# Kernel optimization log

Hardware: AMD Instinct MI355X
Metric: run time of the kernel (lower is better)

## Reference

```python
import jax, jax.numpy as jnp
import numpy as np

N = 50000
E = 500000
IN_DIM = 128
HID = 128
EDGE_DIM = 1
MAX_DEPTH = 4  # depth values in [0, MAX_DEPTH]


def setup_inputs() -> dict:
    key = jax.random.key(0)
    ks = jax.random.split(key, 10)
    x = jax.random.normal(ks[0], (N, IN_DIM), jnp.float32)
    edge_index = jax.random.randint(ks[1], (2, E), 0, N)
    edge_attr = jax.random.normal(ks[2], (E, EDGE_DIM), jnp.float32)
    depth = jax.random.randint(ks[3], (N,), 0, MAX_DEPTH + 1)
    def w(k, sh):
        return (jax.random.normal(k, sh, jnp.float32) / np.float32(np.sqrt(sh[0])))
    return {
        "x": x, "edge_index": edge_index, "edge_attr": edge_attr, "depth": depth,
        "pw": w(ks[4], (IN_DIM, HID)), "pb": jnp.zeros((HID,), jnp.float32),
        "mw1": w(ks[5], (HID + EDGE_DIM, HID)), "mb1": jnp.zeros((HID,), jnp.float32),
        "mw2": w(ks[6], (HID, HID)), "mb2": jnp.zeros((HID,), jnp.float32),
        "uw1": w(ks[7], (2 * HID, HID)), "ub1": jnp.zeros((HID,), jnp.float32),
        "uw2": w(ks[8], (HID, HID)), "ub2": jnp.zeros((HID,), jnp.float32),
    }


def reference(x, edge_index, edge_attr, depth, pw, pb, mw1, mb1, mw2, mb2, uw1, ub1, uw2, ub2):
    src, dst = edge_index[0], edge_index[1]
    dst_depth = depth[dst]  # [E]
    h = x @ pw + pb  # node_proj -> [N, HID]
    # Sequential topological DP over depth levels (static unroll, small count).
    for d in range(1, MAX_DEPTH + 1):
        emask = dst_depth == d  # [E]
        # msg_mlp over all edges using current h (lower-depth nodes already updated)
        msg_in = jnp.concatenate([h[src], edge_attr], axis=-1)  # [E, HID+EDGE_DIM]
        msgs = jax.nn.relu(jax.nn.relu(msg_in @ mw1 + mb1) @ mw2 + mb2)
        msgs = jnp.where(emask[:, None], msgs, jnp.zeros((), h.dtype))
        agg = jax.ops.segment_sum(msgs, dst, num_segments=N)  # [N, HID]
        counts = jax.ops.segment_sum(emask.astype(h.dtype), dst, num_segments=N)
        agg = agg / jnp.clip(counts, 1.0)[:, None]  # mean aggregation, clamp(min=1)
        upd_in = jnp.concatenate([h, agg], axis=-1)  # [N, 2*HID]
        h_new = jax.nn.relu(jax.nn.relu(upd_in @ uw1 + ub1) @ uw2 + ub2)
        h = jnp.where((depth == d)[:, None], h_new, h)
    return h
```

## Files before the change

kernel.cpp:

```cpp
#include <hip/hip_runtime.h>

typedef _Float16 f16;
typedef f16 f16x2 __attribute__((ext_vector_type(2)));
typedef f16 f16x8 __attribute__((ext_vector_type(8)));
typedef float f32x4 __attribute__((ext_vector_type(4)));
typedef float f32x2 __attribute__((ext_vector_type(2)));

#define MFMA16(a, b, c) __builtin_amdgcn_mfma_f32_16x16x32_f16((a), (b), (c), 0, 0, 0)

static __device__ __forceinline__ f16x8 cvt8(const float* __restrict__ p) {
    f32x4 p0 = *(const f32x4*)p;
    f32x4 p1 = *(const f32x4*)(p + 4);
    f16x8 a;
    a[0] = (f16)p0[0]; a[1] = (f16)p0[1]; a[2] = (f16)p0[2]; a[3] = (f16)p0[3];
    a[4] = (f16)p1[0]; a[5] = (f16)p1[1]; a[6] = (f16)p1[2]; a[7] = (f16)p1[3];
    return a;
}

__global__ __launch_bounds__(256) void k_prep(
        const float* __restrict__ pw, const float* __restrict__ mw1,
        const float* __restrict__ mw2, const float* __restrict__ uw1,
        const float* __restrict__ uw2,
        f16* __restrict__ pwp, f16* __restrict__ mw1p, f16* __restrict__ mw2p,
        f16* __restrict__ uw1p, f16* __restrict__ uw2p,
        const int* __restrict__ ei, int* __restrict__ degv,
        const int* __restrict__ dep, int* __restrict__ dcnt,
        int4* __restrict__ recs, int CB, int E, int N) {
    __shared__ int lcnt[4];
    __shared__ int lbase[4];
    int b = blockIdx.x;
    int t = threadIdx.x;
    if (b < 48) {
        const float* W; f16* out; int fb;
        if (b < 8)       { W = pw;  out = pwp;  fb = b; }
        else if (b < 16) { W = mw1; out = mw1p; fb = b - 8; }
        else if (b < 24) { W = mw2; out = mw2p; fb = b - 16; }
        else if (b < 40) { W = uw1; out = uw1p; fb = b - 24; }
        else             { W = uw2; out = uw2p; fb = b - 40; }
        int idx = fb * 256 + t;
        int lane = idx & 63;
        int nt = (idx >> 6) & 7;
        int kt = idx >> 9;
        int colx = lane & 15, quad = lane >> 4;
        f16* o = out + (size_t)idx * 8;
        const float* wb = W + (size_t)(kt * 32 + quad * 8) * 128 + nt * 16 + colx;
#pragma unroll
        for (int j = 0; j < 8; j++) o[j] = (f16)wb[(size_t)j * 128];
    } else if (b < 48 + CB) {
        int e = (b - 48) * 256 + t;
        if (e < E) atomicAdd(&degv[ei[E + e]], 1);
    } else {
        if (t < 4) lcnt[t] = 0;
        __syncthreads();
        int v = (b - 48 - CB) * 256 + t;
        int d = (v < N) ? dep[v] : 0;
        int p = -1;
        if (d >= 1 && d <= 4) p = atomicAdd(&lcnt[d - 1], 1);
        __syncthreads();
        if (t < 4) lbase[t] = (lcnt[t] > 0) ? atomicAdd(&dcnt[t], lcnt[t]) : 0;
        __syncthreads();
        if (d >= 1 && d <= 4) recs[(size_t)(d - 1) * N + lbase[d - 1] + p].x = v;
    }
}

__global__ __launch_bounds__(256) void k_mid(
        const int* __restrict__ degv, int* __restrict__ bsum, int SB,
        const float* __restrict__ x, const f16* __restrict__ pwp,
        const f16* __restrict__ mw1p, const float* __restrict__ pb,
        const float* __restrict__ mb1, float* __restrict__ h,
        f16* __restrict__ hh, f16* __restrict__ t, int N) {
    __shared__ __align__(16) f16 lds[4][16 * 136];
    __shared__ int wsum[4];
    int tid = threadIdx.x;
    if ((int)blockIdx.x < SB) {
        int idx = blockIdx.x * 256 + tid;
        int v = (idx < N) ? degv[idx] : 0;
#pragma unroll
        for (int off = 32; off; off >>= 1) v += __shfl_down(v, off, 64);
        if ((tid & 63) == 0) wsum[tid >> 6] = v;
        __syncthreads();
        if (tid == 0) bsum[blockIdx.x] = wsum[0] + wsum[1] + wsum[2] + wsum[3];
        return;
    }
    int lane = tid & 63, w = tid >> 6;
    int colx = lane & 15, quad = lane >> 4;
    int base = ((blockIdx.x - SB) * 4 + w) * 16;
    int arow = base + colx;
    int u = arow < N ? arow : N - 1;

    f32x4 c1[8];
#pragma unroll
    for (int nt = 0; nt < 8; nt++) c1[nt] = (f32x4){0.f, 0.f, 0.f, 0.f};
#pragma unroll
    for (int kt = 0; kt < 4; kt++) {
        f16x8 a = cvt8(x + (size_t)u * 128 + kt * 32 + quad * 8);
#pragma unroll
        for (int nt = 0; nt < 8; nt++) {
            f16x8 b = *(const f16x8*)(pwp + ((size_t)(kt * 8 + nt) * 64 + lane) * 8);
            c1[nt] = MFMA16(a, b, c1[nt]);
        }
    }
#pragma unroll
    for (int nt = 0; nt < 8; nt++) {
        float bias = pb[nt * 16 + colx];
#pragma unroll
        for (int reg = 0; reg < 4; reg++) {
            int row = quad * 4 + reg;
            int node = base + row;
            float v = c1[nt][reg] + bias;
            lds[w][row * 136 + nt * 16 + colx] = (f16)v;
            if (node < N) {
                h[(size_t)node * 128 + nt * 16 + colx] = v;
                hh[(size_t)node * 128 + nt * 16 + colx] = (f16)v;
            }
        }
    }
    f32x4 c2[8];
#pragma unroll
    for (int nt = 0; nt < 8; nt++) c2[nt] = (f32x4){0.f, 0.f, 0.f, 0.f};
#pragma unroll
    for (int kt = 0; kt < 4; kt++) {
        f16x8 a = *(const f16x8*)&lds[w][colx * 136 + kt * 32 + quad * 8];
#pragma unroll
        for (int nt = 0; nt < 8; nt++) {
            f16x8 b = *(const f16x8*)(mw1p + ((size_t)(kt * 8 + nt) * 64 + lane) * 8);
            c2[nt] = MFMA16(a, b, c2[nt]);
        }
    }
#pragma unroll
    for (int nt = 0; nt < 8; nt++) {
        float bias = mb1[nt * 16 + colx];
#pragma unroll
        for (int reg = 0; reg < 4; reg++) {
            int node = base + quad * 4 + reg;
            if (node < N) t[(size_t)node * 128 + nt * 16 + colx] = (f16)(c2[nt][reg] + bias);
        }
    }
}

__global__ __launch_bounds__(256) void k_scanC(const int* __restrict__ degv,
                                               const int* __restrict__ bsum,
                                               int* __restrict__ rowp, int N, int E) {
    __shared__ int lds[256];
    __shared__ int wo[4];
    int b = blockIdx.x, t = threadIdx.x;
    int idx = b * 256 + t;
    int v = (idx < N) ? degv[idx] : 0;
    lds[t] = v;
    __syncthreads();
#pragma unroll
    for (int d = 1; d < 256; d <<= 1) {
        int u = (t >= d) ? lds[t - d] : 0;
        __syncthreads();
        lds[t] += u;
        __syncthreads();
    }
    int off = 0;
    for (int j = t; j < b; j += 256) off += bsum[j];
#pragma unroll
    for (int o = 32; o; o >>= 1) off += __shfl_down(off, o, 64);
    if ((t & 63) == 0) wo[t >> 6] = off;
    __syncthreads();
    int boff = wo[0] + wo[1] + wo[2] + wo[3];
    if (idx < N) rowp[idx] = boff + lds[t] - v;
    if (b == 0 && t == 0) rowp[N] = E;
}

__global__ __launch_bounds__(256) void k_scat(const int* __restrict__ ei,
                                              const float* __restrict__ eattr,
                                              const int* __restrict__ dep,
                                              const int* __restrict__ rowp,
                                              int* __restrict__ cur,
                                              int2* __restrict__ esea,
                                              int4* __restrict__ recs,
                                              const int* __restrict__ dcnt,
                                              int E, int N) {
    int gtid = blockIdx.x * 256 + threadIdx.x;
    int gsz = gridDim.x * 256;
    for (int e = gtid; e < E; e += gsz) {
        int s = ei[e], d = ei[E + e];
        int p = rowp[d] + atomicAdd(&cur[d], 1);
        esea[p] = (int2){s | (dep[s] << 20), __float_as_int(eattr[e])};
    }
    for (int d4 = 0; d4 < 4; d4++) {
        int cnt = dcnt[d4];
        for (int i = gtid; i < cnt; i += gsz) {
            int4* r = &recs[(size_t)d4 * N + i];
            int u = r->x;
            r->y = rowp[u];
            r->z = rowp[u + 1];
        }
    }
}

__global__ __launch_bounds__(256) void k_md(
        const f16* __restrict__ tOrg, f16* __restrict__ tUpd,
        const float* __restrict__ mw1, const float* __restrict__ mb2,
        const f16* __restrict__ mw2p, const int2* __restrict__ esea,
        const int4* __restrict__ recs, const int* __restrict__ dcnt,
        const f16* __restrict__ hh, const f16* __restrict__ uw1p,
        const f16* __restrict__ uw2p, const f16* __restrict__ mw1p,
        const float* __restrict__ ub1, const float* __restrict__ ub2,
        const float* __restrict__ mb1, float* __restrict__ h,
        int dIdx, int N) {
    __shared__ __align__(16) f16 bsm[128 * 128];
    __shared__ __align__(16) f16 tbuf[4][16][136];
    __shared__ int2 ebuf[4][16];
    __shared__ __align__(16) f16 pool[16][136];
    __shared__ __align__(16) f16 sout[16][136];
    __shared__ int ids[16], se0[16], se1[16];
    {
        const f16x8* s8 = (const f16x8*)mw2p;
        f16x8* d8 = (f16x8*)bsm;
        for (int i = threadIdx.x; i < 2048; i += 256) d8[i] = s8[i];
    }

    const int tid = threadIdx.x;
    const int lane = tid & 63;
    const int w = tid >> 6;
    const int colx = lane & 15, quad = lane >> 4;
    const int cnt = dcnt[dIdx];

    const float* w1r = mw1 + 128 * 128;
    f16x8 w1h[4];
#pragma unroll
    for (int kt = 0; kt < 4; kt++) {
        f32x4 q0 = *(const f32x4*)(w1r + kt * 32 + quad * 8);
        f32x4 q1 = *(const f32x4*)(w1r + kt * 32 + quad * 8 + 4);
        w1h[kt][0] = (f16)q0[0]; w1h[kt][1] = (f16)q0[1];
        w1h[kt][2] = (f16)q0[2]; w1h[kt][3] = (f16)q0[3];
        w1h[kt][4] = (f16)q1[0]; w1h[kt][5] = (f16)q1[1];
        w1h[kt][6] = (f16)q1[2]; w1h[kt][7] = (f16)q1[3];
    }
    float mb2v[8];
#pragma unroll
    for (int nt = 0; nt < 8; nt++) mb2v[nt] = mb2[nt * 16 + colx];

    const int b = blockIdx.x, nb = gridDim.x;
    const int s0 = (int)((long long)cnt * b / nb);
    const int s1 = (int)((long long)cnt * (b + 1) / nb);
    f16* hb = &tbuf[0][0][0];

    __syncthreads();

    for (int cs = s0; cs < s1; cs += 16) {
        int cc = s1 - cs; if (cc > 16) cc = 16;
        if (tid < 16) {
            if (tid < cc) {
                int4 r = recs[(size_t)dIdx * N + cs + tid];
                ids[tid] = r.x; se0[tid] = r.y; se1[tid] = r.z;
            } else {
                ids[tid] = 0; se0[tid] = 0; se1[tid] = 0;
            }
        }
        __syncthreads();

        for (int q = 0; q < 4; q++) {
            int maxT = 0;
#pragma unroll
            for (int s = 0; s < 4; s++) {
                int r = q * 4 + s;
                int tc = (se1[r] - se0[r] + 15) >> 4;
                if (tc > maxT) maxT = tc;
            }
            float aggv[8] = {0.f, 0.f, 0.f, 0.f, 0.f, 0.f, 0.f, 0.f};
            for (int rd = 0; rd < maxT; rd++) {
                if (tid < 64) {
                    int s = tid >> 4, j = tid & 15;
                    int r = q * 4 + s;
                    int es = se0[r] + rd * 16 + j;
                    if (es < se1[r]) ebuf[s][j] = esea[es];
                }
                __syncthreads();
#pragma unroll
                for (int it = 0; it < 4; it++) {
                    int task = it * 256 + tid;
                    int row = task >> 4, seg = task & 15;
                    int s = row >> 4, j = row & 15;
                    int r = q * 4 + s;
                    int es = se0[r] + rd * 16 + j;
                    if (es < se1[r]) {
                        int sv = ebuf[s][j].x;
                        const f16* tb =
                            ((unsigned)((sv >> 20) - 1) < (unsigned)dIdx) ? tUpd : tOrg;
                        *(f16x8*)&tbuf[s][j][seg * 8] =
                            *(const f16x8*)(tb + (size_t)(sv & 0xFFFFF) * 128 + seg * 8);
                    }
                }
                __syncthreads();
                {
                    int r = q * 4 + w;
                    int bs = se0[r] + rd * 16;
                    int rem = se1[r] - bs;
                    if (rem > 0) {
                        f16 eah = (f16)__int_as_float(ebuf[w][colx].y);
                        f16x8 afr[4];
#pragma unroll
                        for (int kt = 0; kt < 4; kt++) {
                            f16x8 v = *(const f16x8*)&tbuf[w][colx][kt * 32 + quad * 8];
                            f16x8 o;
#pragma unroll
                            for (int j2 = 0; j2 < 8; j2++) {
                                f16 qv = v[j2] + eah * w1h[kt][j2];
                                o[j2] = qv > (f16)0 ? qv : (f16)0;
                            }
                            afr[kt] = o;
                        }
#pragma unroll
                        for (int nt = 0; nt < 8; nt++) {
                            f32x4 c = (f32x4){0.f, 0.f, 0.f, 0.f};
#pragma unroll
                            for (int kt = 0; kt < 4; kt++) {
                                f16x8 bb = *(const f16x8*)&bsm[((kt * 8 + nt) * 64 + lane) * 8];
                                c = MFMA16(afr[kt], bb, c);
                            }
#pragma unroll
                            for (int reg = 0; reg < 4; reg++)
                                if (quad * 4 + reg < rem)
                                    aggv[nt] += fmaxf(c[reg] + mb2v[nt], 0.f);
                        }
                    }
                }
                __syncthreads();
            }
            {
                int r = q * 4 + w;
                int deg = se1[r] - se0[r];
                float inv = 1.f / (float)(deg > 1 ? deg : 1);
#pragma unroll
                for (int nt = 0; nt < 8; nt++) {
                    float s = aggv[nt];
                    s += __shfl_xor(s, 16, 64);
                    s += __shfl_xor(s, 32, 64);
                    if (quad == 0) pool[r][nt * 16 + colx] = (f16)(s * inv);
                }
            }
        }
        __syncthreads();

        {
            int row = tid >> 4, seg = tid & 15;
            if (row < cc)
                *(f16x8*)&hb[row * 136 + seg * 8] =
                    *(const f16x8*)(hh + (size_t)ids[row] * 128 + seg * 8);
        }
        __syncthreads();

        f32x4 c1[2];
        c1[0] = (f32x4){0.f, 0.f, 0.f, 0.f};
        c1[1] = (f32x4){0.f, 0.f, 0.f, 0.f};
#pragma unroll
        for (int kt = 0; kt < 8; kt++) {
            f16x8 a;
            if (kt < 4)
                a = *(const f16x8*)&hb[colx * 136 + kt * 32 + quad * 8];
            else
                a = *(const f16x8*)&pool[colx][(kt - 4) * 32 + quad * 8];
#pragma unroll
            for (int j = 0; j < 2; j++) {
                int nt = 2 * w + j;
                f16x8 bb = *(const f16x8*)(uw1p + ((size_t)(kt * 8 + nt) * 64 + lane) * 8);
                c1[j] = MFMA16(a, bb, c1[j]);
            }
        }
#pragma unroll
        for (int j = 0; j < 2; j++) {
            int nt = 2 * w + j;
            float bias = ub1[nt * 16 + colx];
#pragma unroll
            for (int reg = 0; reg < 4; reg++) {
                int row = quad * 4 + reg;
                sout[row][nt * 16 + colx] = (f16)fmaxf(c1[j][reg] + bias, 0.f);
            }
        }
        __syncthreads();
        f32x4 c2[2];
        c2[0] = (f32x4){0.f, 0.f, 0.f, 0.f};
        c2[1] = (f32x4){0.f, 0.f, 0.f, 0.f};
#pragma unroll
        for (int kt = 0; kt < 4; kt++) {
            f16x8 a = *(const f16x8*)&sout[colx][kt * 32 + quad * 8];
#pragma unroll
            for (int j = 0; j < 2; j++) {
                int nt = 2 * w + j;
                f16x8 bb = *(const f16x8*)(uw2p + ((size_t)(kt * 8 + nt) * 64 + lane) * 8);
                c2[j] = MFMA16(a, bb, c2[j]);
            }
        }
#pragma unroll
        for (int j = 0; j < 2; j++) {
            int nt = 2 * w + j;
            float bias = ub2[nt * 16 + colx];
#pragma unroll
            for (int reg = 0; reg < 4; reg++) {
                int row = quad * 4 + reg;
                float v = fmaxf(c2[j][reg] + bias, 0.f);
                pool[row][nt * 16 + colx] = (f16)v;
                if (row < cc)
                    h[(size_t)ids[row] * 128 + nt * 16 + colx] = v;
            }
        }
        __syncthreads();
        if (dIdx < 3) {
            f32x4 c3[2];
            c3[0] = (f32x4){0.f, 0.f, 0.f, 0.f};
            c3[1] = (f32x4){0.f, 0.f, 0.f, 0.f};
#pragma unroll
            for (int kt = 0; kt < 4; kt++) {
                f16x8 a = *(const f16x8*)&pool[colx][kt * 32 + quad * 8];
#pragma unroll
                for (int j = 0; j < 2; j++) {
                    int nt = 2 * w + j;
                    f16x8 bb = *(const f16x8*)(mw1p + ((size_t)(kt * 8 + nt) * 64 + lane) * 8);
                    c3[j] = MFMA16(a, bb, c3[j]);
                }
            }
#pragma unroll
            for (int j = 0; j < 2; j++) {
                int nt = 2 * w + j;
                float bias = mb1[nt * 16 + colx];
#pragma unroll
                for (int reg = 0; reg < 4; reg++) {
                    int row = quad * 4 + reg;
                    if (row < cc)
                        tUpd[(size_t)ids[row] * 128 + nt * 16 + colx] =
                            (f16)(c3[j][reg] + bias);
                }
            }
        }
        __syncthreads();
    }
}

extern "C" void kernel_launch(void* const* d_in, const int* in_sizes, int n_in,
                              void* d_out, int out_size, void* d_ws, size_t ws_size,
                              hipStream_t stream) {
    const float* x    = (const float*)d_in[0];
    const int*   ei   = (const int*)d_in[1];
    const float* eatt = (const float*)d_in[2];
    const int*   dep  = (const int*)d_in[3];
    const float* pw   = (const float*)d_in[4];
    const float* pb   = (const float*)d_in[5];
    const float* mw1  = (const float*)d_in[6];
    const float* mb1  = (const float*)d_in[7];
    const float* mw2  = (const float*)d_in[8];
    const float* mb2  = (const float*)d_in[9];
    const float* uw1  = (const float*)d_in[10];
    const float* ub1  = (const float*)d_in[11];
    const float* uw2  = (const float*)d_in[12];
    const float* ub2  = (const float*)d_in[13];
    float* h = (float*)d_out;

    int N = in_sizes[3];
    int E = in_sizes[1] / 2;
    int NB = (N + 255) / 256;
    int CB = (E + 255) / 256;

    char* ws = (char*)d_ws;
    size_t o = 0;
    auto alloc = [&](size_t bytes) -> char* {
        char* p = ws + o;
        o += (bytes + 255) & ~(size_t)255;
        return p;
    };
    f16*   t    = (f16*)alloc((size_t)N * 128 * 2);
    f16*   hh   = (f16*)alloc((size_t)N * 128 * 2);
    f16*   tUpd = (f16*)alloc((size_t)N * 128 * 2);
    char*  z0   = (char*)alloc(0);
    int*   degv = (int*)alloc((size_t)N * 4);
    int*   cur  = (int*)alloc((size_t)N * 4);
    int*   dcnt = (int*)alloc(64);
    size_t zbytes = (size_t)((char*)alloc(0) - z0);
    int*   rowp = (int*)alloc((size_t)(N + 1) * 4);
    int*   bsum = (int*)alloc((size_t)NB * 4);
    int2*  esea = (int2*)alloc((size_t)E * 8);
    int4*  recs = (int4*)alloc((size_t)4 * N * 16);
    f16*   pwp  = (f16*)alloc(128 * 128 * 2);
    f16*   mw1p = (f16*)alloc(128 * 128 * 2);
    f16*   mw2p = (f16*)alloc(128 * 128 * 2);
    f16*   uw1p = (f16*)alloc(256 * 128 * 2);
    f16*   uw2p = (f16*)alloc(128 * 128 * 2);

    hipMemsetAsync(z0, 0, zbytes, stream);

    k_prep<<<48 + CB + NB, 256, 0, stream>>>(pw, mw1, mw2, uw1, uw2,
                                             pwp, mw1p, mw2p, uw1p, uw2p,
                                             ei, degv, dep, dcnt, recs, CB, E, N);
    int PB = (N + 63) / 64;
    k_mid<<<NB + PB, 256, 0, stream>>>(degv, bsum, NB, x, pwp, mw1p, pb, mb1,
                                       h, hh, t, N);
    k_scanC<<<NB, 256, 0, stream>>>(degv, bsum, rowp, N, E);
    k_scat<<<CB, 256, 0, stream>>>(ei, eatt, dep, rowp, cur, esea, recs, dcnt, E, N);

    for (int d = 0; d < 4; d++) {
        k_md<<<512, 256, 0, stream>>>(t, tUpd, mw1, mb2, mw2p, esea, recs, dcnt,
                                      hh, uw1p, uw2p, mw1p, ub1, ub2, mb1, h,
                                      d, N);
    }
}
```

Measured before the change: 341.9 us.

## Restructure per-depth kernel: 512-thread blocks, batched 16-node edge gather with prefetch

Raises the block size to 512 threads on a 256-block grid. Each chunk of 16 nodes now gathers the first 16 incoming edges of all nodes at once into a 256-row shared tile, and the next chunk's edge records are prefetched while the current one is processed. Node rows for the update MLP are loaded in the same phase, which removes several barriers per round. Edges beyond the first 16 per node are read straight from global memory by each wave, skipping shared staging. The update and message-projection GEMMs are spread over 8 waves instead of 4. This cuts synchronisation and gather latency, at the cost of more shared memory and registers per block, lower occupancy, and uncoalesced global reads for high-degree nodes.

```diff
diff --git a/kernel.cpp b/kernel.cpp
--- a/kernel.cpp
+++ b/kernel.cpp
@@ -193,7 +193,7 @@
     }
 }
 
-__global__ __launch_bounds__(256) void k_md(
+__global__ __launch_bounds__(512) void k_md(
         const f16* __restrict__ tOrg, f16* __restrict__ tUpd,
         const float* __restrict__ mw1, const float* __restrict__ mb2,
         const f16* __restrict__ mw2p, const int2* __restrict__ esea,
@@ -204,22 +204,24 @@
         const float* __restrict__ mb1, float* __restrict__ h,
         int dIdx, int N) {
     __shared__ __align__(16) f16 bsm[128 * 128];
-    __shared__ __align__(16) f16 tbuf[4][16][136];
-    __shared__ int2 ebuf[4][16];
-    __shared__ __align__(16) f16 pool[16][136];
-    __shared__ __align__(16) f16 sout[16][136];
-    __shared__ int ids[16], se0[16], se1[16];
-    {
-        const f16x8* s8 = (const f16x8*)mw2p;
-        f16x8* d8 = (f16x8*)bsm;
-        for (int i = threadIdx.x; i < 2048; i += 256) d8[i] = s8[i];
-    }
+    __shared__ __align__(16) f16 tbuf[256 * 136];
+    __shared__ __align__(16) f16 hbuf[16 * 136];
+    __shared__ __align__(16) f16 pool[16 * 136];
+    __shared__ __align__(16) f16 sout[16 * 136];
+    __shared__ int idsA[64], se0A[64], se1A[64];
 
     const int tid = threadIdx.x;
     const int lane = tid & 63;
     const int w = tid >> 6;
     const int colx = lane & 15, quad = lane >> 4;
     const int cnt = dcnt[dIdx];
+
+    {
+        const f16x8* s8 = (const f16x8*)mw2p;
+        f16x8* d8 = (f16x8*)bsm;
+#pragma unroll
+        for (int i = 0; i < 4; i++) d8[i * 512 + tid] = s8[i * 512 + tid];
+    }
 
     const float* w1r = mw1 + 128 * 128;
     f16x8 w1h[4];
@@ -236,83 +238,134 @@
 #pragma unroll
     for (int nt = 0; nt < 8; nt++) mb2v[nt] = mb2[nt * 16 + colx];
 
+    const int trow = tid & 255;
+    const int thalf = tid >> 8;
+    const int tnode = trow >> 4;
+    const int tj = trow & 15;
+
     const int b = blockIdx.x, nb = gridDim.x;
     const int s0 = (int)((long long)cnt * b / nb);
     const int s1 = (int)((long long)cnt * (b + 1) / nb);
-    f16* hb = &tbuf[0][0][0];
-
-    __syncthreads();
-
-    for (int cs = s0; cs < s1; cs += 16) {
-        int cc = s1 - cs; if (cc > 16) cc = 16;
-        if (tid < 16) {
-            if (tid < cc) {
-                int4 r = recs[(size_t)dIdx * N + cs + tid];
-                ids[tid] = r.x; se0[tid] = r.y; se1[tid] = r.z;
+
+    auto srow = [&](int sv) -> const f16* {
+        const f16* tb = ((unsigned)((sv >> 20) - 1) < (unsigned)dIdx) ? tUpd : tOrg;
+        return tb + (size_t)(sv & 0xFFFFF) * 128;
+    };
+
+    for (int ss = s0; ss < s1; ss += 64) {
+        int scc = s1 - ss; if (scc > 64) scc = 64;
+        __syncthreads();
+        if (tid < 64) {
+            if (tid < scc) {
+                int4 r = recs[(size_t)dIdx * N + ss + tid];
+                idsA[tid] = r.x; se0A[tid] = r.y; se1A[tid] = r.z;
             } else {
-                ids[tid] = 0; se0[tid] = 0; se1[tid] = 0;
-            }
-        }
-        __syncthreads();
-
-        for (int q = 0; q < 4; q++) {
-            int maxT = 0;
-#pragma unroll
-            for (int s = 0; s < 4; s++) {
-                int r = q * 4 + s;
-                int tc = (se1[r] - se0[r] + 15) >> 4;
-                if (tc > maxT) maxT = tc;
-            }
-            float aggv[8] = {0.f, 0.f, 0.f, 0.f, 0.f, 0.f, 0.f, 0.f};
-            for (int rd = 0; rd < maxT; rd++) {
-                if (tid < 64) {
-                    int s = tid >> 4, j = tid & 15;
-                    int r = q * 4 + s;
-                    int es = se0[r] + rd * 16 + j;
-                    if (es < se1[r]) ebuf[s][j] = esea[es];
-                }
-                __syncthreads();
-#pragma unroll
-                for (int it = 0; it < 4; it++) {
-                    int task = it * 256 + tid;
-                    int row = task >> 4, seg = task & 15;
-                    int s = row >> 4, j = row & 15;
-                    int r = q * 4 + s;
-                    int es = se0[r] + rd * 16 + j;
-                    if (es < se1[r]) {
-                        int sv = ebuf[s][j].x;
-                        const f16* tb =
-                            ((unsigned)((sv >> 20) - 1) < (unsigned)dIdx) ? tUpd : tOrg;
-                        *(f16x8*)&tbuf[s][j][seg * 8] =
-                            *(const f16x8*)(tb + (size_t)(sv & 0xFFFFF) * 128 + seg * 8);
+                idsA[tid] = 0; se0A[tid] = 0; se1A[tid] = 0;
+            }
+        }
+        __syncthreads();
+        int nch = (scc + 15) >> 4;
+
+        int2 erec = (int2){0, 0};
+        {
+            int d0 = se1A[tnode] - se0A[tnode];
+            if (tj < d0) erec = esea[se0A[tnode] + tj];
+        }
+
+        for (int ci = 0; ci < nch; ci++) {
+            int cc = scc - ci * 16; if (cc > 16) cc = 16;
+            int gidx = ci * 16 + tnode;
+            int deg = se1A[gidx] - se0A[gidx];
+            bool tval = (tj < deg);
+            f16x8 tld[8];
+            if (tval) {
+                const f16* tr = srow(erec.x) + thalf * 64;
+#pragma unroll
+                for (int i = 0; i < 8; i++) tld[i] = *(const f16x8*)(tr + i * 8);
+            }
+            f16x8 hld;
+            if (tid < 256) {
+                int hrow = tid >> 4, hseg = tid & 15;
+                hld = *(const f16x8*)(hh + (size_t)idsA[ci * 16 + hrow] * 128 + hseg * 8);
+            }
+            int2 erecN = (int2){0, 0};
+            if (ci + 1 < nch) {
+                int g2 = (ci + 1) * 16 + tnode;
+                int d2 = se1A[g2] - se0A[g2];
+                if (tj < d2) erecN = esea[se0A[g2] + tj];
+            }
+            if (tval) {
+                f16* dst = &tbuf[trow * 136 + thalf * 64];
+#pragma unroll
+                for (int i = 0; i < 8; i++) *(f16x8*)(dst + i * 8) = tld[i];
+                if (thalf == 0) tbuf[trow * 136 + 128] = (f16)__int_as_float(erec.y);
+            }
+            if (tid < 256) {
+                int hrow = tid >> 4, hseg = tid & 15;
+                *(f16x8*)&hbuf[hrow * 136 + hseg * 8] = hld;
+            }
+            __syncthreads();
+
+#pragma unroll
+            for (int nn = 0; nn < 2; nn++) {
+                int n = 2 * w + nn;
+                int gi = ci * 16 + n;
+                int nd = se1A[gi] - se0A[gi];
+                float aggv[8] = {0.f, 0.f, 0.f, 0.f, 0.f, 0.f, 0.f, 0.f};
+                if (nd > 0) {
+                    f16 eah = tbuf[(n * 16 + colx) * 136 + 128];
+                    f16x8 afr[4];
+#pragma unroll
+                    for (int kt = 0; kt < 4; kt++) {
+                        f16x8 v = *(const f16x8*)&tbuf[(n * 16 + colx) * 136 + kt * 32 + quad * 8];
+                        f16x8 o;
+#pragma unroll
+                        for (int j2 = 0; j2 < 8; j2++) {
+                            f16 qv = v[j2] + eah * w1h[kt][j2];
+                            o[j2] = qv > (f16)0 ? qv : (f16)0;
+                        }
+                        afr[kt] = o;
                     }
-                }
-                __syncthreads();
-                {
-                    int r = q * 4 + w;
-                    int bs = se0[r] + rd * 16;
-                    int rem = se1[r] - bs;
-                    if (rem > 0) {
-                        f16 eah = (f16)__int_as_float(ebuf[w][colx].y);
-                        f16x8 afr[4];
+                    int rem0 = nd < 16 ? nd : 16;
+#pragma unroll
+                    for (int nt = 0; nt < 8; nt++) {
+                        f32x4 c = (f32x4){0.f, 0.f, 0.f, 0.f};
 #pragma unroll
                         for (int kt = 0; kt < 4; kt++) {
-                            f16x8 v = *(const f16x8*)&tbuf[w][colx][kt * 32 + quad * 8];
+                            f16x8 bb = *(const f16x8*)&bsm[((kt * 8 + nt) * 64 + lane) * 8];
+                            c = MFMA16(afr[kt], bb, c);
+                        }
+#pragma unroll
+                        for (int reg = 0; reg < 4; reg++)
+                            if (quad * 4 + reg < rem0)
+                                aggv[nt] += fmaxf(c[reg] + mb2v[nt], 0.f);
+                    }
+                    for (int bs = 16; bs < nd; bs += 16) {
+                        int lim = se1A[gi] - 1;
+                        int es = se0A[gi] + bs + colx; if (es > lim) es = lim;
+                        int2 er = esea[es];
+                        f16 eah2 = (f16)__int_as_float(er.y);
+                        const f16* trw = srow(er.x);
+                        f16x8 af2[4];
+#pragma unroll
+                        for (int kt = 0; kt < 4; kt++) {
+                            f16x8 v = *(const f16x8*)(trw + kt * 32 + quad * 8);
                             f16x8 o;
 #pragma unroll
                             for (int j2 = 0; j2 < 8; j2++) {
-                                f16 qv = v[j2] + eah * w1h[kt][j2];
+                                f16 qv = v[j2] + eah2 * w1h[kt][j2];
                                 o[j2] = qv > (f16)0 ? qv : (f16)0;
                             }
-                            afr[kt] = o;
+                            af2[kt] = o;
                         }
+                        int rem = nd - bs;
 #pragma unroll
                         for (int nt = 0; nt < 8; nt++) {
                             f32x4 c = (f32x4){0.f, 0.f, 0.f, 0.f};
 #pragma unroll
                             for (int kt = 0; kt < 4; kt++) {
                                 f16x8 bb = *(const f16x8*)&bsm[((kt * 8 + nt) * 64 + lane) * 8];
-                                c = MFMA16(afr[kt], bb, c);
+                                c = MFMA16(af2[kt], bb, c);
                             }
 #pragma unroll
                             for (int reg = 0; reg < 4; reg++)
@@ -321,114 +374,76 @@
                         }
                     }
                 }
-                __syncthreads();
-            }
-            {
-                int r = q * 4 + w;
-                int deg = se1[r] - se0[r];
-                float inv = 1.f / (float)(deg > 1 ? deg : 1);
+                float inv = 1.f / (float)(nd > 1 ? nd : 1);
 #pragma unroll
                 for (int nt = 0; nt < 8; nt++) {
                     float s = aggv[nt];
                     s += __shfl_xor(s, 16, 64);
                     s += __shfl_xor(s, 32, 64);
-                    if (quad == 0) pool[r][nt * 16 + colx] = (f16)(s * inv);
+                    if (quad == 0) pool[n * 136 + nt * 16 + colx] = (f16)(s * inv);
                 }
             }
-        }
-        __syncthreads();
-
-        {
-            int row = tid >> 4, seg = tid & 15;
-            if (row < cc)
-                *(f16x8*)&hb[row * 136 + seg * 8] =
-                    *(const f16x8*)(hh + (size_t)ids[row] * 128 + seg * 8);
-        }
-        __syncthreads();
-
-        f32x4 c1[2];
-        c1[0] = (f32x4){0.f, 0.f, 0.f, 0.f};
-        c1[1] = (f32x4){0.f, 0.f, 0.f, 0.f};
-#pragma unroll
-        for (int kt = 0; kt < 8; kt++) {
-            f16x8 a;
-            if (kt < 4)
-                a = *(const f16x8*)&hb[colx * 136 + kt * 32 + quad * 8];
-            else
-                a = *(const f16x8*)&pool[colx][(kt - 4) * 32 + quad * 8];
-#pragma unroll
-            for (int j = 0; j < 2; j++) {
-                int nt = 2 * w + j;
-                f16x8 bb = *(const f16x8*)(uw1p + ((size_t)(kt * 8 + nt) * 64 + lane) * 8);
-                c1[j] = MFMA16(a, bb, c1[j]);
-            }
-        }
-#pragma unroll
-        for (int j = 0; j < 2; j++) {
-            int nt = 2 * w + j;
-            float bias = ub1[nt * 16 + colx];
-#pragma unroll
-            for (int reg = 0; reg < 4; reg++) {
-                int row = quad * 4 + reg;
-                sout[row][nt * 16 + colx] = (f16)fmaxf(c1[j][reg] + bias, 0.f);
-            }
-        }
-        __syncthreads();
-        f32x4 c2[2];
-        c2[0] = (f32x4){0.f, 0.f, 0.f, 0.f};
-        c2[1] = (f32x4){0.f, 0.f, 0.f, 0.f};
-#pragma unroll
-        for (int kt = 0; kt < 4; kt++) {
-            f16x8 a = *(const f16x8*)&sout[colx][kt * 32 + quad * 8];
-#pragma unroll
-            for (int j = 0; j < 2; j++) {
-                int nt = 2 * w + j;
-                f16x8 bb = *(const f16x8*)(uw2p + ((size_t)(kt * 8 + nt) * 64 + lane) * 8);
-                c2[j] = MFMA16(a, bb, c2[j]);
-            }
-        }
-#pragma unroll
-        for (int j = 0; j < 2; j++) {
-            int nt = 2 * w + j;
-            float bias = ub2[nt * 16 + colx];
-#pragma unroll
-            for (int reg = 0; reg < 4; reg++) {
-                int row = quad * 4 + reg;
-                float v = fmaxf(c2[j][reg] + bias, 0.f);
-                pool[row][nt * 16 + colx] = (f16)v;
-                if (row < cc)
-                    h[(size_t)ids[row] * 128 + nt * 16 + colx] = v;
-            }
-        }
-        __syncthreads();
-        if (dIdx < 3) {
-            f32x4 c3[2];
-            c3[0] = (f32x4){0.f, 0.f, 0.f, 0.f};
-            c3[1] = (f32x4){0.f, 0.f, 0.f, 0.f};
+            __syncthreads();
+
+            f32x4 c1 = (f32x4){0.f, 0.f, 0.f, 0.f};
+#pragma unroll
+            for (int kt = 0; kt < 8; kt++) {
+                f16x8 a;
+                if (kt < 4)
+                    a = *(const f16x8*)&hbuf[colx * 136 + kt * 32 + quad * 8];
+                else
+                    a = *(const f16x8*)&pool[colx * 136 + (kt - 4) * 32 + quad * 8];
+                f16x8 bb = *(const f16x8*)(uw1p + ((size_t)(kt * 8 + w) * 64 + lane) * 8);
+                c1 = MFMA16(a, bb, c1);
+            }
+            {
+                float bias = ub1[w * 16 + colx];
+#pragma unroll
+                for (int reg = 0; reg < 4; reg++) {
+                    int row = quad * 4 + reg;
+                    sout[row * 136 + w * 16 + colx] = (f16)fmaxf(c1[reg] + bias, 0.f);
+                }
+            }
+            __syncthreads();
+            f32x4 c2 = (f32x4){0.f, 0.f, 0.f, 0.f};
 #pragma unroll
             for (int kt = 0; kt < 4; kt++) {
-                f16x8 a = *(const f16x8*)&pool[colx][kt * 32 + quad * 8];
-#pragma unroll
-                for (int j = 0; j < 2; j++) {
-                    int nt = 2 * w + j;
-                    f16x8 bb = *(const f16x8*)(mw1p + ((size_t)(kt * 8 + nt) * 64 + lane) * 8);
-                    c3[j] = MFMA16(a, bb, c3[j]);
+                f16x8 a = *(const f16x8*)&sout[colx * 136 + kt * 32 + quad * 8];
+                f16x8 bb = *(const f16x8*)(uw2p + ((size_t)(kt * 8 + w) * 64 + lane) * 8);
+                c2 = MFMA16(a, bb, c2);
+            }
+            {
+                float bias = ub2[w * 16 + colx];
+#pragma unroll
+                for (int reg = 0; reg < 4; reg++) {
+                    int row = quad * 4 + reg;
+                    float v = fmaxf(c2[reg] + bias, 0.f);
+                    pool[row * 136 + w * 16 + colx] = (f16)v;
+                    if (row < cc)
+                        h[(size_t)idsA[ci * 16 + row] * 128 + w * 16 + colx] = v;
                 }
             }
-#pragma unroll
-            for (int j = 0; j < 2; j++) {
-                int nt = 2 * w + j;
-                float bias = mb1[nt * 16 + colx];
+            __syncthreads();
+            if (dIdx < 3) {
+                f32x4 c3 = (f32x4){0.f, 0.f, 0.f, 0.f};
+#pragma unroll
+                for (int kt = 0; kt < 4; kt++) {
+                    f16x8 a = *(const f16x8*)&pool[colx * 136 + kt * 32 + quad * 8];
+                    f16x8 bb = *(const f16x8*)(mw1p + ((size_t)(kt * 8 + w) * 64 + lane) * 8);
+                    c3 = MFMA16(a, bb, c3);
+                }
+                float bias = mb1[w * 16 + colx];
 #pragma unroll
                 for (int reg = 0; reg < 4; reg++) {
                     int row = quad * 4 + reg;
                     if (row < cc)
-                        tUpd[(size_t)ids[row] * 128 + nt * 16 + colx] =
-                            (f16)(c3[j][reg] + bias);
+                        tUpd[(size_t)idsA[ci * 16 + row] * 128 + w * 16 + colx] =
+                            (f16)(c3[reg] + bias);
                 }
             }
-        }
-        __syncthreads();
+            __syncthreads();
+            erec = erecN;
+        }
     }
 }
 
@@ -493,7 +508,7 @@
     k_scat<<<CB, 256, 0, stream>>>(ei, eatt, dep, rowp, cur, esea, recs, dcnt, E, N);
 
     for (int d = 0; d < 4; d++) {
-        k_md<<<512, 256, 0, stream>>>(t, tUpd, mw1, mb2, mw2p, esea, recs, dcnt,
+        k_md<<<256, 512, 0, stream>>>(t, tUpd, mw1, mb2, mw2p, esea, recs, dcnt,
                                       hh, uw1p, uw2p, mw1p, ub1, ub2, mb1, h,
                                       d, N);
     }
```

Measured after the change: 470.1 us. 1.37x slower.

## Register-prefetch next node group's source rows and drop per-round edge syncs

Applied to the files above, without the earlier changes.

Restructures the message-aggregation loop in the depth kernel. Edge records for all 16 nodes of a chunk are loaded up front. Source-row gathers for the next group of four nodes are issued into registers while the current group computes, and then committed to a double-buffered LDS tile. Nodes with more than 16 edges now have each wave load its own extra rows directly from global memory, with no block barriers, which removes the old per-round maxT loop and its three __syncthreads. The LDS padding changes from 136 to 132 and sout shares space with the tile buffer. The cost is higher register pressure, and the overflow edges use uncoalesced direct loads.

```diff
diff --git a/kernel.cpp b/kernel.cpp
--- a/kernel.cpp
+++ b/kernel.cpp
@@ -204,22 +204,26 @@
         const float* __restrict__ mb1, float* __restrict__ h,
         int dIdx, int N) {
     __shared__ __align__(16) f16 bsm[128 * 128];
-    __shared__ __align__(16) f16 tbuf[4][16][136];
-    __shared__ int2 ebuf[4][16];
-    __shared__ __align__(16) f16 pool[16][136];
-    __shared__ __align__(16) f16 sout[16][136];
+    __shared__ __align__(16) f16 tbuf[2][4][16][132];
+    __shared__ __align__(16) f16 pool[16][132];
+    __shared__ int2 ebuf[16][16];
     __shared__ int ids[16], se0[16], se1[16];
-    {
-        const f16x8* s8 = (const f16x8*)mw2p;
-        f16x8* d8 = (f16x8*)bsm;
-        for (int i = threadIdx.x; i < 2048; i += 256) d8[i] = s8[i];
-    }
+    f16* hbuf = &tbuf[0][0][0][0];
+    f16* sout = &tbuf[1][0][0][0];
 
     const int tid = threadIdx.x;
     const int lane = tid & 63;
     const int w = tid >> 6;
     const int colx = lane & 15, quad = lane >> 4;
+    const int er0 = tid >> 4;
+    const int sg = tid & 15;
     const int cnt = dcnt[dIdx];
+
+    {
+        const f16x8* s8 = (const f16x8*)mw2p;
+        f16x8* d8 = (f16x8*)bsm;
+        for (int i = tid; i < 2048; i += 256) d8[i] = s8[i];
+    }
 
     const float* w1r = mw1 + 128 * 128;
     f16x8 w1h[4];
@@ -237,14 +241,33 @@
     for (int nt = 0; nt < 8; nt++) mb2v[nt] = mb2[nt * 16 + colx];
 
     const int b = blockIdx.x, nb = gridDim.x;
-    const int s0 = (int)((long long)cnt * b / nb);
-    const int s1 = (int)((long long)cnt * (b + 1) / nb);
-    f16* hb = &tbuf[0][0][0];
+    const int s0g = (int)((long long)cnt * b / nb);
+    const int s1g = (int)((long long)cnt * (b + 1) / nb);
+
+    auto srow = [&](int sv) -> const f16* {
+        const f16* tb = ((unsigned)((sv >> 20) - 1) < (unsigned)dIdx) ? tUpd : tOrg;
+        return tb + (size_t)(sv & 0xFFFFF) * 128;
+    };
+
+#define ISSUE1(dst, qq, it)                                                    \
+    do {                                                                       \
+        int nn_ = (qq) * 4 + (it);                                             \
+        if (er0 < se1[nn_] - se0[nn_]) {                                       \
+            int sv_ = ebuf[nn_][er0].x;                                        \
+            dst = *(const f16x8*)(srow(sv_) + sg * 8);                         \
+        }                                                                      \
+    } while (0)
+#define COMMIT1(src, qq, it)                                                   \
+    do {                                                                       \
+        int nn_ = (qq) * 4 + (it);                                             \
+        if (er0 < se1[nn_] - se0[nn_])                                         \
+            *(f16x8*)&tbuf[(qq) & 1][it][er0][sg * 8] = src;                   \
+    } while (0)
 
     __syncthreads();
 
-    for (int cs = s0; cs < s1; cs += 16) {
-        int cc = s1 - cs; if (cc > 16) cc = 16;
+    for (int cs = s0g; cs < s1g; cs += 16) {
+        int cc = s1g - cs; if (cc > 16) cc = 16;
         if (tid < 16) {
             if (tid < cc) {
                 int4 r = recs[(size_t)dIdx * N + cs + tid];
@@ -254,96 +277,101 @@
             }
         }
         __syncthreads();
-
+        {
+            int dg = se1[er0] - se0[er0];
+            if (sg < dg) ebuf[er0][sg] = esea[se0[er0] + sg];
+        }
+        __syncthreads();
+
+        f16x8 sr0{}, sr1{}, sr2{}, sr3{};
+        ISSUE1(sr0, 0, 0); ISSUE1(sr1, 0, 1); ISSUE1(sr2, 0, 2); ISSUE1(sr3, 0, 3);
         for (int q = 0; q < 4; q++) {
-            int maxT = 0;
-#pragma unroll
-            for (int s = 0; s < 4; s++) {
-                int r = q * 4 + s;
-                int tc = (se1[r] - se0[r] + 15) >> 4;
-                if (tc > maxT) maxT = tc;
-            }
+            COMMIT1(sr0, q, 0); COMMIT1(sr1, q, 1);
+            COMMIT1(sr2, q, 2); COMMIT1(sr3, q, 3);
+            if (q < 3) {
+                ISSUE1(sr0, q + 1, 0); ISSUE1(sr1, q + 1, 1);
+                ISSUE1(sr2, q + 1, 2); ISSUE1(sr3, q + 1, 3);
+            }
+            __syncthreads();
+
+            int n = q * 4 + w;
+            int nd = se1[n] - se0[n];
             float aggv[8] = {0.f, 0.f, 0.f, 0.f, 0.f, 0.f, 0.f, 0.f};
-            for (int rd = 0; rd < maxT; rd++) {
-                if (tid < 64) {
-                    int s = tid >> 4, j = tid & 15;
-                    int r = q * 4 + s;
-                    int es = se0[r] + rd * 16 + j;
-                    if (es < se1[r]) ebuf[s][j] = esea[es];
+            if (nd > 0) {
+                f16 eah = (f16)__int_as_float(ebuf[n][colx].y);
+                f16x8 afr[4];
+#pragma unroll
+                for (int kt = 0; kt < 4; kt++) {
+                    f16x8 v = *(const f16x8*)&tbuf[q & 1][w][colx][kt * 32 + quad * 8];
+                    f16x8 o;
+#pragma unroll
+                    for (int j2 = 0; j2 < 8; j2++) {
+                        f16 qv = v[j2] + eah * w1h[kt][j2];
+                        o[j2] = qv > (f16)0 ? qv : (f16)0;
+                    }
+                    afr[kt] = o;
                 }
-                __syncthreads();
-#pragma unroll
-                for (int it = 0; it < 4; it++) {
-                    int task = it * 256 + tid;
-                    int row = task >> 4, seg = task & 15;
-                    int s = row >> 4, j = row & 15;
-                    int r = q * 4 + s;
-                    int es = se0[r] + rd * 16 + j;
-                    if (es < se1[r]) {
-                        int sv = ebuf[s][j].x;
-                        const f16* tb =
-                            ((unsigned)((sv >> 20) - 1) < (unsigned)dIdx) ? tUpd : tOrg;
-                        *(f16x8*)&tbuf[s][j][seg * 8] =
-                            *(const f16x8*)(tb + (size_t)(sv & 0xFFFFF) * 128 + seg * 8);
+                int rem0 = nd < 16 ? nd : 16;
+#pragma unroll
+                for (int nt = 0; nt < 8; nt++) {
+                    f32x4 c = (f32x4){0.f, 0.f, 0.f, 0.f};
+#pragma unroll
+                    for (int kt = 0; kt < 4; kt++) {
+                        f16x8 bb = *(const f16x8*)&bsm[((kt * 8 + nt) * 64 + lane) * 8];
+                        c = MFMA16(afr[kt], bb, c);
+                    }
+#pragma unroll
+                    for (int reg = 0; reg < 4; reg++)
+                        if (quad * 4 + reg < rem0)
+                            aggv[nt] += fmaxf(c[reg] + mb2v[nt], 0.f);
+                }
+                for (int bs = 16; bs < nd; bs += 16) {
+                    int lim = se1[n] - 1;
+                    int es = se0[n] + bs + colx; if (es > lim) es = lim;
+                    int2 er = esea[es];
+                    f16 eah2 = (f16)__int_as_float(er.y);
+                    const f16* trw = srow(er.x);
+                    f16x8 af2[4];
+#pragma unroll
+                    for (int kt = 0; kt < 4; kt++) {
+                        f16x8 v = *(const f16x8*)(trw + kt * 32 + quad * 8);
+                        f16x8 o;
+#pragma unroll
+                        for (int j2 = 0; j2 < 8; j2++) {
+                            f16 qv = v[j2] + eah2 * w1h[kt][j2];
+                            o[j2] = qv > (f16)0 ? qv : (f16)0;
+                        }
+                        af2[kt] = o;
+                    }
+                    int rem = nd - bs;
+#pragma unroll
+                    for (int nt = 0; nt < 8; nt++) {
+                        f32x4 c = (f32x4){0.f, 0.f, 0.f, 0.f};
+#pragma unroll
+                        for (int kt = 0; kt < 4; kt++) {
+                            f16x8 bb = *(const f16x8*)&bsm[((kt * 8 + nt) * 64 + lane) * 8];
+                            c = MFMA16(af2[kt], bb, c);
+                        }
+#pragma unroll
+                        for (int reg = 0; reg < 4; reg++)
+                            if (quad * 4 + reg < rem)
+                                aggv[nt] += fmaxf(c[reg] + mb2v[nt], 0.f);
                     }
                 }
-                __syncthreads();
-                {
-                    int r = q * 4 + w;
-                    int bs = se0[r] + rd * 16;
-                    int rem = se1[r] - bs;
-                    if (rem > 0) {
-                        f16 eah = (f16)__int_as_float(ebuf[w][colx].y);
-                        f16x8 afr[4];
-#pragma unroll
-                        for (int kt = 0; kt < 4; kt++) {
-                            f16x8 v = *(const f16x8*)&tbuf[w][colx][kt * 32 + quad * 8];
-                            f16x8 o;
-#pragma unroll
-                            for (int j2 = 0; j2 < 8; j2++) {
-                                f16 qv = v[j2] + eah * w1h[kt][j2];
-                                o[j2] = qv > (f16)0 ? qv : (f16)0;
-                            }
-                            afr[kt] = o;
-                        }
-#pragma unroll
-                        for (int nt = 0; nt < 8; nt++) {
-                            f32x4 c = (f32x4){0.f, 0.f, 0.f, 0.f};
-#pragma unroll
-                            for (int kt = 0; kt < 4; kt++) {
-                                f16x8 bb = *(const f16x8*)&bsm[((kt * 8 + nt) * 64 + lane) * 8];
-                                c = MFMA16(afr[kt], bb, c);
-                            }
-#pragma unroll
-                            for (int reg = 0; reg < 4; reg++)
-                                if (quad * 4 + reg < rem)
-                                    aggv[nt] += fmaxf(c[reg] + mb2v[nt], 0.f);
-                        }
-                    }
-                }
-                __syncthreads();
-            }
-            {
-                int r = q * 4 + w;
-                int deg = se1[r] - se0[r];
-                float inv = 1.f / (float)(deg > 1 ? deg : 1);
-#pragma unroll
-                for (int nt = 0; nt < 8; nt++) {
-                    float s = aggv[nt];
-                    s += __shfl_xor(s, 16, 64);
-                    s += __shfl_xor(s, 32, 64);
-                    if (quad == 0) pool[r][nt * 16 + colx] = (f16)(s * inv);
-                }
-            }
-        }
-        __syncthreads();
-
-        {
-            int row = tid >> 4, seg = tid & 15;
-            if (row < cc)
-                *(f16x8*)&hb[row * 136 + seg * 8] =
-                    *(const f16x8*)(hh + (size_t)ids[row] * 128 + seg * 8);
-        }
+            }
+            float inv = 1.f / (float)(nd > 1 ? nd : 1);
+#pragma unroll
+            for (int nt = 0; nt < 8; nt++) {
+                float s = aggv[nt];
+                s += __shfl_xor(s, 16, 64);
+                s += __shfl_xor(s, 32, 64);
+                if (quad == 0) pool[n][nt * 16 + colx] = (f16)(s * inv);
+            }
+        }
+        __syncthreads();
+
+        *(f16x8*)&hbuf[er0 * 132 + sg * 8] =
+            *(const f16x8*)(hh + (size_t)ids[er0] * 128 + sg * 8);
         __syncthreads();
 
         f32x4 c1[2];
@@ -353,7 +381,7 @@
         for (int kt = 0; kt < 8; kt++) {
             f16x8 a;
             if (kt < 4)
-                a = *(const f16x8*)&hb[colx * 136 + kt * 32 + quad * 8];
+                a = *(const f16x8*)&hbuf[colx * 132 + kt * 32 + quad * 8];
             else
                 a = *(const f16x8*)&pool[colx][(kt - 4) * 32 + quad * 8];
 #pragma unroll
@@ -370,7 +398,7 @@
 #pragma unroll
             for (int reg = 0; reg < 4; reg++) {
                 int row = quad * 4 + reg;
-                sout[row][nt * 16 + colx] = (f16)fmaxf(c1[j][reg] + bias, 0.f);
+                sout[row * 132 + nt * 16 + colx] = (f16)fmaxf(c1[j][reg] + bias, 0.f);
             }
         }
         __syncthreads();
@@ -379,7 +407,7 @@
         c2[1] = (f32x4){0.f, 0.f, 0.f, 0.f};
 #pragma unroll
         for (int kt = 0; kt < 4; kt++) {
-            f16x8 a = *(const f16x8*)&sout[colx][kt * 32 + quad * 8];
+            f16x8 a = *(const f16x8*)&sout[colx * 132 + kt * 32 + quad * 8];
 #pragma unroll
             for (int j = 0; j < 2; j++) {
                 int nt = 2 * w + j;
@@ -430,6 +458,8 @@
         }
         __syncthreads();
     }
+#undef ISSUE1
+#undef COMMIT1
 }
 
 extern "C" void kernel_launch(void* const* d_in, const int* in_sizes, int n_in,
```

Result: slower. 397.6 us (+16.3%).

## Double k_md block to 512 threads, eight waves processing eight nodes per round

Applied to the files above, without the earlier changes.

Widens the per-depth message/update kernel from 4 to 8 waves per block. Each round now gathers edge rows for 8 destination nodes at once (two groups instead of four), and each wave in the update MLPs computes a single 16-column tile instead of two. The aim is more memory-level parallelism in the gather and shorter serial chains per block. In exchange it raises LDS use per block and register pressure under a 512-thread bound, and padding rows are now loaded unconditionally from ids index 0.

```diff
diff --git a/kernel.cpp b/kernel.cpp
--- a/kernel.cpp
+++ b/kernel.cpp
@@ -193,7 +193,7 @@
     }
 }
 
-__global__ __launch_bounds__(256) void k_md(
+__global__ __launch_bounds__(512) void k_md(
         const f16* __restrict__ tOrg, f16* __restrict__ tUpd,
         const float* __restrict__ mw1, const float* __restrict__ mb2,
         const f16* __restrict__ mw2p, const int2* __restrict__ esea,
@@ -204,22 +204,25 @@
         const float* __restrict__ mb1, float* __restrict__ h,
         int dIdx, int N) {
     __shared__ __align__(16) f16 bsm[128 * 128];
-    __shared__ __align__(16) f16 tbuf[4][16][136];
-    __shared__ int2 ebuf[4][16];
+    __shared__ __align__(16) f16 tbuf[8][16][136];
     __shared__ __align__(16) f16 pool[16][136];
     __shared__ __align__(16) f16 sout[16][136];
+    __shared__ int2 ebuf[8][16];
     __shared__ int ids[16], se0[16], se1[16];
-    {
-        const f16x8* s8 = (const f16x8*)mw2p;
-        f16x8* d8 = (f16x8*)bsm;
-        for (int i = threadIdx.x; i < 2048; i += 256) d8[i] = s8[i];
-    }
+    f16* hbuf = &tbuf[0][0][0];
 
     const int tid = threadIdx.x;
     const int lane = tid & 63;
     const int w = tid >> 6;
     const int colx = lane & 15, quad = lane >> 4;
     const int cnt = dcnt[dIdx];
+
+    {
+        const f16x8* s8 = (const f16x8*)mw2p;
+        f16x8* d8 = (f16x8*)bsm;
+#pragma unroll
+        for (int i = 0; i < 4; i++) d8[i * 512 + tid] = s8[i * 512 + tid];
+    }
 
     const float* w1r = mw1 + 128 * 128;
     f16x8 w1h[4];
@@ -239,7 +242,11 @@
     const int b = blockIdx.x, nb = gridDim.x;
     const int s0 = (int)((long long)cnt * b / nb);
     const int s1 = (int)((long long)cnt * (b + 1) / nb);
-    f16* hb = &tbuf[0][0][0];
+
+    auto srow = [&](int sv) -> const f16* {
+        const f16* tb = ((unsigned)((sv >> 20) - 1) < (unsigned)dIdx) ? tUpd : tOrg;
+        return tb + (size_t)(sv & 0xFFFFF) * 128;
+    };
 
     __syncthreads();
 
@@ -255,41 +262,39 @@
         }
         __syncthreads();
 
-        for (int q = 0; q < 4; q++) {
+        for (int g = 0; g < 2; g++) {
             int maxT = 0;
 #pragma unroll
-            for (int s = 0; s < 4; s++) {
-                int r = q * 4 + s;
+            for (int s = 0; s < 8; s++) {
+                int r = g * 8 + s;
                 int tc = (se1[r] - se0[r] + 15) >> 4;
                 if (tc > maxT) maxT = tc;
             }
             float aggv[8] = {0.f, 0.f, 0.f, 0.f, 0.f, 0.f, 0.f, 0.f};
             for (int rd = 0; rd < maxT; rd++) {
-                if (tid < 64) {
+                if (tid < 128) {
                     int s = tid >> 4, j = tid & 15;
-                    int r = q * 4 + s;
+                    int r = g * 8 + s;
                     int es = se0[r] + rd * 16 + j;
                     if (es < se1[r]) ebuf[s][j] = esea[es];
                 }
                 __syncthreads();
 #pragma unroll
                 for (int it = 0; it < 4; it++) {
-                    int task = it * 256 + tid;
+                    int task = it * 512 + tid;
                     int row = task >> 4, seg = task & 15;
                     int s = row >> 4, j = row & 15;
-                    int r = q * 4 + s;
+                    int r = g * 8 + s;
                     int es = se0[r] + rd * 16 + j;
                     if (es < se1[r]) {
                         int sv = ebuf[s][j].x;
-                        const f16* tb =
-                            ((unsigned)((sv >> 20) - 1) < (unsigned)dIdx) ? tUpd : tOrg;
                         *(f16x8*)&tbuf[s][j][seg * 8] =
-                            *(const f16x8*)(tb + (size_t)(sv & 0xFFFFF) * 128 + seg * 8);
+                            *(const f16x8*)(srow(sv) + seg * 8);
                     }
                 }
                 __syncthreads();
                 {
-                    int r = q * 4 + w;
+                    int r = g * 8 + w;
                     int bs = se0[r] + rd * 16;
                     int rem = se1[r] - bs;
                     if (rem > 0) {
@@ -324,7 +329,7 @@
                 __syncthreads();
             }
             {
-                int r = q * 4 + w;
+                int r = g * 8 + w;
                 int deg = se1[r] - se0[r];
                 float inv = 1.f / (float)(deg > 1 ? deg : 1);
 #pragma unroll
@@ -338,94 +343,67 @@
         }
         __syncthreads();
 
-        {
+        if (tid < 256) {
             int row = tid >> 4, seg = tid & 15;
-            if (row < cc)
-                *(f16x8*)&hb[row * 136 + seg * 8] =
-                    *(const f16x8*)(hh + (size_t)ids[row] * 128 + seg * 8);
-        }
-        __syncthreads();
-
-        f32x4 c1[2];
-        c1[0] = (f32x4){0.f, 0.f, 0.f, 0.f};
-        c1[1] = (f32x4){0.f, 0.f, 0.f, 0.f};
+            *(f16x8*)&hbuf[row * 136 + seg * 8] =
+                *(const f16x8*)(hh + (size_t)ids[row] * 128 + seg * 8);
+        }
+        __syncthreads();
+
+        f32x4 c1 = (f32x4){0.f, 0.f, 0.f, 0.f};
 #pragma unroll
         for (int kt = 0; kt < 8; kt++) {
             f16x8 a;
             if (kt < 4)
-                a = *(const f16x8*)&hb[colx * 136 + kt * 32 + quad * 8];
+                a = *(const f16x8*)&hbuf[colx * 136 + kt * 32 + quad * 8];
             else
                 a = *(const f16x8*)&pool[colx][(kt - 4) * 32 + quad * 8];
-#pragma unroll
-            for (int j = 0; j < 2; j++) {
-                int nt = 2 * w + j;
-                f16x8 bb = *(const f16x8*)(uw1p + ((size_t)(kt * 8 + nt) * 64 + lane) * 8);
-                c1[j] = MFMA16(a, bb, c1[j]);
-            }
-        }
-#pragma unroll
-        for (int j = 0; j < 2; j++) {
-            int nt = 2 * w + j;
-            float bias = ub1[nt * 16 + colx];
+            f16x8 bb = *(const f16x8*)(uw1p + ((size_t)(kt * 8 + w) * 64 + lane) * 8);
+            c1 = MFMA16(a, bb, c1);
+        }
+        {
+            float bias = ub1[w * 16 + colx];
 #pragma unroll
             for (int reg = 0; reg < 4; reg++) {
                 int row = quad * 4 + reg;
-                sout[row][nt * 16 + colx] = (f16)fmaxf(c1[j][reg] + bias, 0.f);
-            }
-        }
-        __syncthreads();
-        f32x4 c2[2];
-        c2[0] = (f32x4){0.f, 0.f, 0.f, 0.f};
-        c2[1] = (f32x4){0.f, 0.f, 0.f, 0.f};
+                sout[row][w * 16 + colx] = (f16)fmaxf(c1[reg] + bias, 0.f);
+            }
+        }
+        __syncthreads();
+        f32x4 c2 = (f32x4){0.f, 0.f, 0.f, 0.f};
 #pragma unroll
         for (int kt = 0; kt < 4; kt++) {
             f16x8 a = *(const f16x8*)&sout[colx][kt * 32 + quad * 8];
-#pragma unroll
-            for (int j = 0; j < 2; j++) {
-                int nt = 2 * w + j;
-                f16x8 bb = *(const f16x8*)(uw2p + ((size_t)(kt * 8 + nt) * 64 + lane) * 8);
-                c2[j] = MFMA16(a, bb, c2[j]);
-            }
-        }
-#pragma unroll
-        for (int j = 0; j < 2; j++) {
-            int nt = 2 * w + j;
-            float bias = ub2[nt * 16 + colx];
+            f16x8 bb = *(const f16x8*)(uw2p + ((size_t)(kt * 8 + w) * 64 + lane) * 8);
+            c2 = MFMA16(a, bb, c2);
+        }
+        {
+            float bias = ub2[w * 16 + colx];
 #pragma unroll
             for (int reg = 0; reg < 4; reg++) {
                 int row = quad * 4 + reg;
-                float v = fmaxf(c2[j][reg] + bias, 0.f);
-                pool[row][nt * 16 + colx] = (f16)v;
+                float v = fmaxf(c2[reg] + bias, 0.f);
+                pool[row][w * 16 + colx] = (f16)v;
                 if (row < cc)
-                    h[(size_t)ids[row] * 128 + nt * 16 + colx] = v;
+                    h[(size_t)ids[row] * 128 + w * 16 + colx] = v;
             }
         }
         __syncthreads();
         if (dIdx < 3) {
-            f32x4 c3[2];
-            c3[0] = (f32x4){0.f, 0.f, 0.f, 0.f};
-            c3[1] = (f32x4){0.f, 0.f, 0.f, 0.f};
+            f32x4 c3 = (f32x4){0.f, 0.f, 0.f, 0.f};
 #pragma unroll
             for (int kt = 0; kt < 4; kt++) {
                 f16x8 a = *(const f16x8*)&pool[colx][kt * 32 + quad * 8];
-#pragma unroll
-                for (int j = 0; j < 2; j++) {
-                    int nt = 2 * w + j;
-                    f16x8 bb = *(const f16x8*)(mw1p + ((size_t)(kt * 8 + nt) * 64 + lane) * 8);
-                    c3[j] = MFMA16(a, bb, c3[j]);
-                }
-            }
-#pragma unroll
-            for (int j = 0; j < 2; j++) {
-                int nt = 2 * w + j;
-                float bias = mb1[nt * 16 + colx];
-#pragma unroll
-                for (int reg = 0; reg < 4; reg++) {
-                    int row = quad * 4 + reg;
-                    if (row < cc)
-                        tUpd[(size_t)ids[row] * 128 + nt * 16 + colx] =
-                            (f16)(c3[j][reg] + bias);
-                }
+                f16x8 bb = *(const f16x8*)(mw1p + ((size_t)(kt * 8 + w) * 64 + lane) * 8);
+                c3 = MFMA16(a, bb, c3);
+            }
+            float bias = mb1[w * 16 + colx];
+#pragma unroll
+            for (int reg = 0; reg < 4; reg++) {
+                int row = quad * 4 + reg;
+                if (row < cc)
+                    tUpd[(size_t)ids[row] * 128 + w * 16 + colx] =
+                        (f16)(c3[reg] + bias);
             }
         }
         __syncthreads();
@@ -493,7 +471,7 @@
     k_scat<<<CB, 256, 0, stream>>>(ei, eatt, dep, rowp, cur, esea, recs, dcnt, E, N);
 
     for (int d = 0; d < 4; d++) {
-        k_md<<<512, 256, 0, stream>>>(t, tUpd, mw1, mb2, mw2p, esea, recs, dcnt,
+        k_md<<<512, 512, 0, stream>>>(t, tUpd, mw1, mb2, mw2p, esea, recs, dcnt,
                                       hh, uw1p, uw2p, mw1p, ub1, ub2, mb1, h,
                                       d, N);
     }
```

New measurement: 345.7 us. Within noise of the previous version (+1.1%).
